# Optimization experiments

Hardware: AMD Instinct MI355X
Metric: run time of the kernel (lower is better)

## Reference

```python
import jax, jax.numpy as jnp
import numpy as np

S, B, D = 256, 256, 512
H, M = 512, 512

def setup_inputs() -> dict:
    key = jax.random.key(0)
    ks = jax.random.split(key, 5)
    scale = 0.05
    return {
        "input": jax.random.normal(ks[0], (S, B, D), dtype=jnp.float32),
        "w_ih": jax.random.normal(ks[1], (3 * H, D), dtype=jnp.float32) * scale,
        "w_hh": jax.random.normal(ks[2], (3 * H, H), dtype=jnp.float32) * scale,
        "b_ih": jnp.zeros((3 * H,), dtype=jnp.float32),
        "b_hh": jnp.zeros((3 * H,), dtype=jnp.float32),
        "W1": jax.random.normal(ks[3], (M, H), dtype=jnp.float32) * scale,
        "b1": jnp.zeros((M,), dtype=jnp.float32),
        "W2": jax.random.normal(ks[4], (1, M), dtype=jnp.float32) * scale,
        "b2": jnp.zeros((1,), dtype=jnp.float32),
    }

def _gru_cell(x_t, h, w_ih, w_hh, b_ih, b_hh):
    # PyTorch GRUCell: gates ordered (r, z, n) along the 3H axis.
    gi = x_t @ w_ih.T + b_ih            # [B, 3H]
    gh = h @ w_hh.T + b_hh              # [B, 3H]
    i_r, i_z, i_n = jnp.split(gi, 3, axis=-1)
    h_r, h_z, h_n = jnp.split(gh, 3, axis=-1)
    r = jax.nn.sigmoid(i_r + h_r)
    z = jax.nn.sigmoid(i_z + h_z)
    n = jnp.tanh(i_n + r * h_n)
    return (1.0 - z) * n + z * h

def reference(input, w_ih, w_hh, b_ih, b_hh, W1, b1, W2, b2):
    seq_len, batch_size, _ = input.shape
    h0 = jnp.zeros((batch_size, w_hh.shape[1]), dtype=input.dtype)

    def step(h, x_t):
        h_new = _gru_cell(x_t, h, w_ih, w_hh, b_ih, b_hh)
        return h_new, None

    h_final, _ = jax.lax.scan(step, h0, input)
    out1 = jnp.tanh(h_final @ W1.T + b1)   # [B, M]
    value = jnp.tanh(out1 @ W2.T + b2)     # [B, 1]
    return value
```

## Files before the change

### kernel.cpp

```cpp
#include <hip/hip_runtime.h>
#include <hip/hip_bf16.h>

typedef __attribute__((ext_vector_type(8))) short short8v;
typedef __attribute__((ext_vector_type(4))) float f32x4;

union SV { short8v v; unsigned short u[8]; };
union FU { float f; unsigned u; };
union QF { unsigned long long q[4]; float4 v[2]; };

__device__ __forceinline__ void split2(float x, unsigned short& hi, unsigned short& lo) {
    FU a; a.f = x;
    hi = (unsigned short)(a.u >> 16);
    FU h; h.u = a.u & 0xffff0000u;
    FU r; r.f = x - h.f;
    lo = (unsigned short)(r.u >> 16);
}
__device__ __forceinline__ void split8(const float4 a0, const float4 a1, SV& h, SV& l) {
    split2(a0.x, h.u[0], l.u[0]); split2(a0.y, h.u[1], l.u[1]);
    split2(a0.z, h.u[2], l.u[2]); split2(a0.w, h.u[3], l.u[3]);
    split2(a1.x, h.u[4], l.u[4]); split2(a1.y, h.u[5], l.u[5]);
    split2(a1.z, h.u[6], l.u[6]); split2(a1.w, h.u[7], l.u[7]);
}
__device__ __forceinline__ float sigmoidf_(float x) {
    return 1.0f / (1.0f + __expf(-x));
}

__device__ __forceinline__ unsigned long long h_load64(const float* p) {
    return __hip_atomic_load((const unsigned long long*)p,
                             __ATOMIC_RELAXED, __HIP_MEMORY_SCOPE_AGENT);
}
__device__ __forceinline__ float h_load32(const float* p) {
    FU u; u.u = __hip_atomic_load((const unsigned*)p,
                                  __ATOMIC_RELAXED, __HIP_MEMORY_SCOPE_AGENT);
    return u.f;
}
__device__ __forceinline__ void h_store32(float* p, float v) {
    FU u; u.f = v;
    __hip_atomic_store((unsigned*)p, u.u,
                       __ATOMIC_RELAXED, __HIP_MEMORY_SCOPE_AGENT);
}

__device__ __forceinline__ void group_barrier(unsigned* gf, const int ct,
                                              const unsigned gen) {
    __builtin_amdgcn_s_waitcnt(0);
    __syncthreads();
    __atomic_signal_fence(__ATOMIC_SEQ_CST);
    if (threadIdx.x == 0)
        __hip_atomic_store(&gf[ct], gen,
                           __ATOMIC_RELAXED, __HIP_MEMORY_SCOPE_AGENT);
    if (threadIdx.x < 16) {
        const unsigned long long* f64 = (const unsigned long long*)gf;
        for (;;) {
            unsigned long long v = __hip_atomic_load(
                &f64[threadIdx.x], __ATOMIC_RELAXED, __HIP_MEMORY_SCOPE_AGENT);
            if (((unsigned)v >= gen) && ((unsigned)(v >> 32) >= gen)) break;
            __builtin_amdgcn_s_sleep(1);
        }
    }
    __atomic_signal_fence(__ATOMIC_SEQ_CST);
    __syncthreads();
}

__global__ __launch_bounds__(256) void cast_split(
    const float* __restrict__ in, unsigned short* __restrict__ hi,
    unsigned short* __restrict__ lo, int n4)
{
    int i = blockIdx.x * 256 + threadIdx.x;
    if (i < n4) {
        float4 v = ((const float4*)in)[i];
        ushort4 h, l;
        split2(v.x, h.x, l.x); split2(v.y, h.y, l.y);
        split2(v.z, h.z, l.z); split2(v.w, h.w, l.w);
        ((ushort4*)hi)[i] = h;
        ((ushort4*)lo)[i] = l;
    }
}

__global__ __launch_bounds__(256, 2) void gemm_gi_mfma(
    const float* __restrict__ A,
    const unsigned short* __restrict__ Bh,
    const unsigned short* __restrict__ Bl,
    const float* __restrict__ bias,
    float* __restrict__ C)
{
    __shared__ __attribute__((aligned(16))) unsigned char lds[65536];
    const int t = threadIdx.x;
    const int l = t & 63, w = t >> 6;
    const int nb = blockIdx.x, mb = blockIdx.y;
    const int p = t & 7;
    const int rbase = t >> 3;
    f32x4 acc[4][4] = {};

    for (int kk = 0; kk < 512; kk += 64) {
#pragma unroll
        for (int i = 0; i < 4; ++i) {
            const int r = i * 32 + rbase;
            const int q = p ^ (r & 7);
            const float* ga = A + (size_t)(mb * 128 + r) * 512 + kk + q * 8;
            SV ah, al;
            split8(*(const float4*)ga, *(const float4*)(ga + 4), ah, al);
            const int o = r * 128 + p * 16;
            *(short8v*)&lds[o] = ah.v;
            *(short8v*)&lds[16384 + o] = al.v;
            const size_t gb = (size_t)(nb * 128 + r) * 512 + kk + q * 8;
            *(short8v*)&lds[32768 + o] = *(const short8v*)(Bh + gb);
            *(short8v*)&lds[49152 + o] = *(const short8v*)(Bl + gb);
        }
        __syncthreads();
        const int mr0 = (w >> 1) * 64, nc0 = (w & 1) * 64;
#pragma unroll
        for (int kk2 = 0; kk2 < 2; ++kk2) {
            const int kap = kk2 * 4 + (l >> 4);
            short8v ah[4], al[4], bh[4], bl[4];
#pragma unroll
            for (int i = 0; i < 4; ++i) {
                const int row = mr0 + i * 16 + (l & 15);
                const int off = row * 128 + ((kap ^ (row & 7)) * 16);
                ah[i] = *(const short8v*)&lds[off];
                al[i] = *(const short8v*)&lds[16384 + off];
            }
#pragma unroll
            for (int j = 0; j < 4; ++j) {
                const int bn = nc0 + j * 16 + (l & 15);
                const int off = bn * 128 + ((kap ^ (bn & 7)) * 16);
                bh[j] = *(const short8v*)&lds[32768 + off];
                bl[j] = *(const short8v*)&lds[49152 + off];
            }
#pragma unroll
            for (int i = 0; i < 4; ++i)
#pragma unroll
                for (int j = 0; j < 4; ++j) {
                    acc[i][j] = __builtin_amdgcn_mfma_f32_16x16x32_bf16(ah[i], bh[j], acc[i][j], 0, 0, 0);
                    acc[i][j] = __builtin_amdgcn_mfma_f32_16x16x32_bf16(ah[i], bl[j], acc[i][j], 0, 0, 0);
                    acc[i][j] = __builtin_amdgcn_mfma_f32_16x16x32_bf16(al[i], bh[j], acc[i][j], 0, 0, 0);
                }
        }
        __syncthreads();
    }
    const int mr0 = (w >> 1) * 64, nc0 = (w & 1) * 64;
#pragma unroll
    for (int j = 0; j < 4; ++j) {
        const int col = nb * 128 + nc0 + j * 16 + (l & 15);
        const float bv = bias[col];
#pragma unroll
        for (int i = 0; i < 4; ++i) {
            const int row0 = mb * 128 + mr0 + i * 16 + (l >> 4) * 4;
#pragma unroll
            for (int rg = 0; rg < 4; ++rg)
                C[(size_t)(row0 + rg) * 1536 + col] = acc[i][j][rg] + bv;
        }
    }
}

__device__ __forceinline__ void gru_tile_body(
    float* accs_f,
    const float* __restrict__ gi_s,
    const unsigned short* __restrict__ whhH,
    const unsigned short* __restrict__ whhL,
    const float* __restrict__ bhh,
    const float* __restrict__ hold,
    float* __restrict__ hnew,
    const int tid, const int rt, const int ct)
{
    const int l = tid & 63, wv = tid >> 6;
    const int c0 = ct * 16, row0 = rt * 16;
    const int arow = l & 15;
    const int ksl  = l >> 4;
    const int kbase = wv * 128;

    unsigned long long a_raw[4][4];
    const float* ha = hold + (size_t)(row0 + arow) * 512 + kbase + ksl * 8;
#pragma unroll
    for (int j = 0; j < 4; ++j)
#pragma unroll
        for (int q = 0; q < 4; ++q)
            a_raw[j][q] = h_load64(ha + j * 32 + q * 2);

    f32x4 acc[3] = {};
#pragma unroll
    for (int j = 0; j < 4; ++j) {
        QF buf;
#pragma unroll
        for (int q = 0; q < 4; ++q) buf.q[q] = a_raw[j][q];
        SV ah, al;
        split8(buf.v[0], buf.v[1], ah, al);
        const int ko = kbase + j * 32 + ksl * 8;
#pragma unroll
        for (int g = 0; g < 3; ++g) {
            const size_t wo = (size_t)((g << 9) + c0 + arow) * 512 + ko;
            const short8v bh = *(const short8v*)(whhH + wo);
            const short8v bl = *(const short8v*)(whhL + wo);
            acc[g] = __builtin_amdgcn_mfma_f32_16x16x32_bf16(ah.v, bh, acc[g], 0, 0, 0);
            acc[g] = __builtin_amdgcn_mfma_f32_16x16x32_bf16(ah.v, bl, acc[g], 0, 0, 0);
            acc[g] = __builtin_amdgcn_mfma_f32_16x16x32_bf16(al.v, bh, acc[g], 0, 0, 0);
        }
    }

#pragma unroll
    for (int g = 0; g < 3; ++g)
#pragma unroll
        for (int rg = 0; rg < 4; ++rg)
            accs_f[((wv * 3 + g) * 4 + rg) * 64 + l] = acc[g][rg];
    __syncthreads();

    const int col = c0 + arow;
    const int row = row0 + ((l >> 4) << 2) + wv;
    float s0 = accs_f[((0 * 3 + 0) * 4 + wv) * 64 + l]
             + accs_f[((1 * 3 + 0) * 4 + wv) * 64 + l]
             + accs_f[((2 * 3 + 0) * 4 + wv) * 64 + l]
             + accs_f[((3 * 3 + 0) * 4 + wv) * 64 + l];
    float s1 = accs_f[((0 * 3 + 1) * 4 + wv) * 64 + l]
             + accs_f[((1 * 3 + 1) * 4 + wv) * 64 + l]
             + accs_f[((2 * 3 + 1) * 4 + wv) * 64 + l]
             + accs_f[((3 * 3 + 1) * 4 + wv) * 64 + l];
    float s2 = accs_f[((0 * 3 + 2) * 4 + wv) * 64 + l]
             + accs_f[((1 * 3 + 2) * 4 + wv) * 64 + l]
             + accs_f[((2 * 3 + 2) * 4 + wv) * 64 + l]
             + accs_f[((3 * 3 + 2) * 4 + wv) * 64 + l];
    const float* gp = gi_s + (size_t)row * 1536 + col;
    const float hv = h_load32(hold + (size_t)row * 512 + col);
    const float r = sigmoidf_(gp[0]    + s0 + bhh[col]);
    const float z = sigmoidf_(gp[512]  + s1 + bhh[512 + col]);
    const float n = tanhf(gp[1024] + r * (s2 + bhh[1024 + col]));
    h_store32(hnew + (size_t)row * 512 + col, (1.0f - z) * n + z * hv);
    __syncthreads();
}

__global__ __launch_bounds__(256, 2) void gru_coop(
    const float* __restrict__ gi,
    const unsigned short* __restrict__ whhH,
    const unsigned short* __restrict__ whhL,
    const float* __restrict__ bhh,
    float* __restrict__ hA, float* __restrict__ hB,
    unsigned* __restrict__ flags,
    const int t0, const int tc)
{
    __shared__ float accs_f[4 * 3 * 4 * 64];
    const int tid = threadIdx.x;
    const int ct = blockIdx.x & 31;
    const int rt = blockIdx.x >> 5;
    unsigned* gf = flags + rt * 32;
    for (int s = 0; s < tc; ++s) {
        const int t = t0 + s;
        const float* hold = (t & 1) ? hB : hA;
        float* hnew = (t & 1) ? hA : hB;
        gru_tile_body(accs_f, gi + (size_t)s * 256 * 1536, whhH, whhL, bhh,
                      hold, hnew, tid, rt, ct);
        if (s + 1 < tc)
            group_barrier(gf, ct, (unsigned)(t + 1));
    }
}

__global__ __launch_bounds__(256, 2) void gru_step_fb(
    const float* __restrict__ gi_s,
    const unsigned short* __restrict__ whhH,
    const unsigned short* __restrict__ whhL,
    const float* __restrict__ bhh,
    const float* __restrict__ hold, float* __restrict__ hnew)
{
    __shared__ float accs_f[4 * 3 * 4 * 64];
    gru_tile_body(accs_f, gi_s, whhH, whhL, bhh, hold, hnew,
                  threadIdx.x, blockIdx.x >> 5, blockIdx.x & 31);
}

template<bool TANH>
__global__ __launch_bounds__(256) void gemm_nt_bias(
    const float* __restrict__ A, const float* __restrict__ B,
    const float* __restrict__ bias, float* __restrict__ C,
    const int N, const int K)
{
    __shared__ float As[32][68];
    __shared__ float Bs[32][68];
    const int nb = blockIdx.x, mb = blockIdx.y;
    const int t  = threadIdx.x;
    const int tx = t & 15, ty = t >> 4;
    const int lr = t >> 3;
    const int lk = (t & 7) << 2;
    const float* pA = A + (size_t)(mb * 64 + lr) * K + lk;
    const float* pB = B + (size_t)(nb * 64 + lr) * K + lk;
    float acc[4][4];
#pragma unroll
    for (int i = 0; i < 4; ++i)
#pragma unroll
        for (int j = 0; j < 4; ++j) acc[i][j] = 0.0f;
    for (int kk = 0; kk < K; kk += 32) {
        const float4 a0 = *(const float4*)(pA + kk);
        const float4 a1 = *(const float4*)(pA + (size_t)32 * K + kk);
        const float4 b0 = *(const float4*)(pB + kk);
        const float4 b1 = *(const float4*)(pB + (size_t)32 * K + kk);
        __syncthreads();
        As[lk+0][lr] = a0.x; As[lk+1][lr] = a0.y; As[lk+2][lr] = a0.z; As[lk+3][lr] = a0.w;
        As[lk+0][lr+32] = a1.x; As[lk+1][lr+32] = a1.y; As[lk+2][lr+32] = a1.z; As[lk+3][lr+32] = a1.w;
        Bs[lk+0][lr] = b0.x; Bs[lk+1][lr] = b0.y; Bs[lk+2][lr] = b0.z; Bs[lk+3][lr] = b0.w;
        Bs[lk+0][lr+32] = b1.x; Bs[lk+1][lr+32] = b1.y; Bs[lk+2][lr+32] = b1.z; Bs[lk+3][lr+32] = b1.w;
        __syncthreads();
#pragma unroll
        for (int k = 0; k < 32; ++k) {
            const float4 av = *(const float4*)&As[k][ty << 2];
            const float4 bv = *(const float4*)&Bs[k][tx << 2];
            acc[0][0] += av.x * bv.x; acc[0][1] += av.x * bv.y; acc[0][2] += av.x * bv.z; acc[0][3] += av.x * bv.w;
            acc[1][0] += av.y * bv.x; acc[1][1] += av.y * bv.y; acc[1][2] += av.y * bv.z; acc[1][3] += av.y * bv.w;
            acc[2][0] += av.z * bv.x; acc[2][1] += av.z * bv.y; acc[2][2] += av.z * bv.z; acc[2][3] += av.z * bv.w;
            acc[3][0] += av.w * bv.x; acc[3][1] += av.w * bv.y; acc[3][2] += av.w * bv.z; acc[3][3] += av.w * bv.w;
        }
    }
    const int crow = mb * 64 + (ty << 2);
    const int ccol = nb * 64 + (tx << 2);
    const float4 bv = *(const float4*)(bias + ccol);
#pragma unroll
    for (int i = 0; i < 4; ++i) {
        float4 o;
        o.x = acc[i][0] + bv.x; o.y = acc[i][1] + bv.y;
        o.z = acc[i][2] + bv.z; o.w = acc[i][3] + bv.w;
        if (TANH) { o.x = tanhf(o.x); o.y = tanhf(o.y); o.z = tanhf(o.z); o.w = tanhf(o.w); }
        *(float4*)(C + (size_t)(crow + i) * N + ccol) = o;
    }
}

__global__ __launch_bounds__(256) void value_head(
    const float* __restrict__ out1, const float* __restrict__ W2,
    const float* __restrict__ b2, float* __restrict__ out)
{
    const int b = blockIdx.x, t = threadIdx.x;
    float p = out1[(size_t)b * 512 + t] * W2[t]
            + out1[(size_t)b * 512 + 256 + t] * W2[256 + t];
#pragma unroll
    for (int off = 32; off > 0; off >>= 1) p += __shfl_down(p, off, 64);
    __shared__ float ps[4];
    if ((t & 63) == 0) ps[t >> 6] = p;
    __syncthreads();
    if (t == 0) out[b] = tanhf(ps[0] + ps[1] + ps[2] + ps[3] + b2[0]);
}

extern "C" void kernel_launch(void* const* d_in, const int* in_sizes, int n_in,
                              void* d_out, int out_size, void* d_ws, size_t ws_size,
                              hipStream_t stream)
{
    (void)in_sizes; (void)n_in; (void)out_size;
    const float* input = (const float*)d_in[0];
    const float* w_ih  = (const float*)d_in[1];
    const float* w_hh  = (const float*)d_in[2];
    const float* b_ih  = (const float*)d_in[3];
    const float* b_hh  = (const float*)d_in[4];
    const float* W1    = (const float*)d_in[5];
    const float* b1    = (const float*)d_in[6];
    const float* W2    = (const float*)d_in[7];
    const float* b2    = (const float*)d_in[8];
    float* out = (float*)d_out;
    float* ws  = (float*)d_ws;

    float* hA = ws;
    float* hB = ws + 131072;
    float* o1 = ws + 262144;
    unsigned short* wihH = (unsigned short*)(ws + 393216);
    unsigned short* wihL = (unsigned short*)(ws + 786432);
    unsigned short* whhH = (unsigned short*)(ws + 1179648);
    unsigned short* whhL = (unsigned short*)(ws + 1572864);
    unsigned* flags = (unsigned*)(ws + 1966080);
    float* gi = ws + 1966592;

    const size_t per_step = 256 * 1536;
    const size_t base = 1966592;
    const size_t avail = (ws_size / 4 > base) ? ws_size / 4 - base : 0;
    int Tc = (int)(avail / per_step);
    if (Tc > 256) Tc = 256;
    if (Tc < 1) Tc = 1;

    hipMemsetAsync(hA, 0, 131072 * sizeof(float), stream);
    hipMemsetAsync(flags, 0, 512 * sizeof(unsigned), stream);

    cast_split<<<768, 256, 0, stream>>>(w_ih, wihH, wihL, 196608);
    cast_split<<<768, 256, 0, stream>>>(w_hh, whhH, whhL, 196608);

    for (int t0 = 0; t0 < 256; t0 += Tc) {
        const int tc = (t0 + Tc <= 256) ? Tc : (256 - t0);
        const int Mc = tc * 256;
        gemm_gi_mfma<<<dim3(12, Mc / 128), 256, 0, stream>>>(
            input + (size_t)t0 * 256 * 512, wihH, wihL, b_ih, gi);
        {
            const float* a_gi = gi;
            const unsigned short* a_wh = whhH; const unsigned short* a_wl = whhL;
            const float* a_bh = b_hh;
            float* a_hA = hA; float* a_hB = hB;
            unsigned* a_fl = flags;
            int a_t0 = t0; int a_tc = tc;
            void* args[] = {&a_gi, &a_wh, &a_wl, &a_bh, &a_hA, &a_hB, &a_fl, &a_t0, &a_tc};
            hipError_t rc = hipLaunchCooperativeKernel(
                (const void*)gru_coop, dim3(512), dim3(256), args, 0, stream);
            if (rc != hipSuccess) {
                for (int s = 0; s < tc; ++s) {
                    const int t = t0 + s;
                    const float* hold = (t & 1) ? hB : hA;
                    float* hnew = (t & 1) ? hA : hB;
                    gru_step_fb<<<dim3(512), 256, 0, stream>>>(
                        gi + (size_t)s * per_step, whhH, whhL, b_hh, hold, hnew);
                }
            }
        }
    }

    gemm_nt_bias<true><<<dim3(512 / 64, 256 / 64), 256, 0, stream>>>(
        hA, W1, b1, o1, 512, 512);
    value_head<<<256, 256, 0, stream>>>(o1, W2, b2, out);
}
```

Baseline: 2.476 ms.

## Fuse input projection into cooperative GRU kernel, overlapping with the step barrier

Removes the separate gi GEMM and its large global gi buffer. The cooperative recurrent kernel now computes each tile's input-gate projection for step t+1 itself, right after writing h for step t and before waiting on the group barrier, so this independent work fills the barrier wait. It drops the gi write and read round trip through HBM but loses the efficient LDS-tiled GEMM. W_ih is now re-read every step from global memory, and each block performs extra MFMA work inside the serial loop.

```diff
diff --git a/kernel.cpp b/kernel.cpp
--- a/kernel.cpp
+++ b/kernel.cpp
@@ -76,97 +76,68 @@
     }
 }
 
-__global__ __launch_bounds__(256, 2) void gemm_gi_mfma(
-    const float* __restrict__ A,
-    const unsigned short* __restrict__ Bh,
-    const unsigned short* __restrict__ Bl,
-    const float* __restrict__ bias,
-    float* __restrict__ C)
-{
-    __shared__ __attribute__((aligned(16))) unsigned char lds[65536];
-    const int t = threadIdx.x;
-    const int l = t & 63, w = t >> 6;
-    const int nb = blockIdx.x, mb = blockIdx.y;
-    const int p = t & 7;
-    const int rbase = t >> 3;
-    f32x4 acc[4][4] = {};
-
-    for (int kk = 0; kk < 512; kk += 64) {
-#pragma unroll
-        for (int i = 0; i < 4; ++i) {
-            const int r = i * 32 + rbase;
-            const int q = p ^ (r & 7);
-            const float* ga = A + (size_t)(mb * 128 + r) * 512 + kk + q * 8;
-            SV ah, al;
-            split8(*(const float4*)ga, *(const float4*)(ga + 4), ah, al);
-            const int o = r * 128 + p * 16;
-            *(short8v*)&lds[o] = ah.v;
-            *(short8v*)&lds[16384 + o] = al.v;
-            const size_t gb = (size_t)(nb * 128 + r) * 512 + kk + q * 8;
-            *(short8v*)&lds[32768 + o] = *(const short8v*)(Bh + gb);
-            *(short8v*)&lds[49152 + o] = *(const short8v*)(Bl + gb);
-        }
-        __syncthreads();
-        const int mr0 = (w >> 1) * 64, nc0 = (w & 1) * 64;
-#pragma unroll
-        for (int kk2 = 0; kk2 < 2; ++kk2) {
-            const int kap = kk2 * 4 + (l >> 4);
-            short8v ah[4], al[4], bh[4], bl[4];
-#pragma unroll
-            for (int i = 0; i < 4; ++i) {
-                const int row = mr0 + i * 16 + (l & 15);
-                const int off = row * 128 + ((kap ^ (row & 7)) * 16);
-                ah[i] = *(const short8v*)&lds[off];
-                al[i] = *(const short8v*)&lds[16384 + off];
-            }
-#pragma unroll
-            for (int j = 0; j < 4; ++j) {
-                const int bn = nc0 + j * 16 + (l & 15);
-                const int off = bn * 128 + ((kap ^ (bn & 7)) * 16);
-                bh[j] = *(const short8v*)&lds[32768 + off];
-                bl[j] = *(const short8v*)&lds[49152 + off];
-            }
-#pragma unroll
-            for (int i = 0; i < 4; ++i)
-#pragma unroll
-                for (int j = 0; j < 4; ++j) {
-                    acc[i][j] = __builtin_amdgcn_mfma_f32_16x16x32_bf16(ah[i], bh[j], acc[i][j], 0, 0, 0);
-                    acc[i][j] = __builtin_amdgcn_mfma_f32_16x16x32_bf16(ah[i], bl[j], acc[i][j], 0, 0, 0);
-                    acc[i][j] = __builtin_amdgcn_mfma_f32_16x16x32_bf16(al[i], bh[j], acc[i][j], 0, 0, 0);
-                }
-        }
-        __syncthreads();
-    }
-    const int mr0 = (w >> 1) * 64, nc0 = (w & 1) * 64;
+__device__ __forceinline__ void gi_compute(
+    float* accs_g,
+    const float* __restrict__ X,
+    const unsigned short* __restrict__ wihH,
+    const unsigned short* __restrict__ wihL,
+    const int step, const int tid, const int rt, const int ct,
+    const float bir, const float biz, const float bin,
+    float& gr, float& gz, float& gn)
+{
+    const int l = tid & 63, wv = tid >> 6;
+    const int arow = l & 15, ksl = l >> 4, kbase = wv * 128;
+    const int c0 = ct * 16, row0 = rt * 16;
+    const float* xa = X + ((size_t)step * 256 + row0 + arow) * 512 + kbase + ksl * 8;
+    f32x4 acc[3] = {};
 #pragma unroll
     for (int j = 0; j < 4; ++j) {
-        const int col = nb * 128 + nc0 + j * 16 + (l & 15);
-        const float bv = bias[col];
-#pragma unroll
-        for (int i = 0; i < 4; ++i) {
-            const int row0 = mb * 128 + mr0 + i * 16 + (l >> 4) * 4;
-#pragma unroll
-            for (int rg = 0; rg < 4; ++rg)
-                C[(size_t)(row0 + rg) * 1536 + col] = acc[i][j][rg] + bv;
-        }
-    }
-}
-
-__device__ __forceinline__ void gru_tile_body(
-    float* accs_f,
-    const float* __restrict__ gi_s,
+        const float4 x0 = *(const float4*)(xa + j * 32);
+        const float4 x1 = *(const float4*)(xa + j * 32 + 4);
+        SV ah, al;
+        split8(x0, x1, ah, al);
+        const int ko = kbase + j * 32 + ksl * 8;
+#pragma unroll
+        for (int g = 0; g < 3; ++g) {
+            const size_t wo = (size_t)((g << 9) + c0 + arow) * 512 + ko;
+            const short8v bh = *(const short8v*)(wihH + wo);
+            const short8v bl = *(const short8v*)(wihL + wo);
+            acc[g] = __builtin_amdgcn_mfma_f32_16x16x32_bf16(ah.v, bh, acc[g], 0, 0, 0);
+            acc[g] = __builtin_amdgcn_mfma_f32_16x16x32_bf16(ah.v, bl, acc[g], 0, 0, 0);
+            acc[g] = __builtin_amdgcn_mfma_f32_16x16x32_bf16(al.v, bh, acc[g], 0, 0, 0);
+        }
+    }
+#pragma unroll
+    for (int g = 0; g < 3; ++g)
+#pragma unroll
+        for (int rg = 0; rg < 4; ++rg)
+            accs_g[((wv * 3 + g) * 4 + rg) * 64 + l] = acc[g][rg];
+    __syncthreads();
+    gr = accs_g[((0 * 3 + 0) * 4 + wv) * 64 + l]
+       + accs_g[((1 * 3 + 0) * 4 + wv) * 64 + l]
+       + accs_g[((2 * 3 + 0) * 4 + wv) * 64 + l]
+       + accs_g[((3 * 3 + 0) * 4 + wv) * 64 + l] + bir;
+    gz = accs_g[((0 * 3 + 1) * 4 + wv) * 64 + l]
+       + accs_g[((1 * 3 + 1) * 4 + wv) * 64 + l]
+       + accs_g[((2 * 3 + 1) * 4 + wv) * 64 + l]
+       + accs_g[((3 * 3 + 1) * 4 + wv) * 64 + l] + biz;
+    gn = accs_g[((0 * 3 + 2) * 4 + wv) * 64 + l]
+       + accs_g[((1 * 3 + 2) * 4 + wv) * 64 + l]
+       + accs_g[((2 * 3 + 2) * 4 + wv) * 64 + l]
+       + accs_g[((3 * 3 + 2) * 4 + wv) * 64 + l] + bin;
+}
+
+__device__ __forceinline__ void recur_compute(
+    float* accs_r,
     const unsigned short* __restrict__ whhH,
     const unsigned short* __restrict__ whhL,
-    const float* __restrict__ bhh,
     const float* __restrict__ hold,
-    float* __restrict__ hnew,
-    const int tid, const int rt, const int ct)
+    const int tid, const int rt, const int ct,
+    float& s0, float& s1, float& s2)
 {
     const int l = tid & 63, wv = tid >> 6;
+    const int arow = l & 15, ksl = l >> 4, kbase = wv * 128;
     const int c0 = ct * 16, row0 = rt * 16;
-    const int arow = l & 15;
-    const int ksl  = l >> 4;
-    const int kbase = wv * 128;
 
     unsigned long long a_raw[4][4];
     const float* ha = hold + (size_t)(row0 + arow) * 512 + kbase + ksl * 8;
@@ -195,72 +166,106 @@
             acc[g] = __builtin_amdgcn_mfma_f32_16x16x32_bf16(al.v, bh, acc[g], 0, 0, 0);
         }
     }
-
 #pragma unroll
     for (int g = 0; g < 3; ++g)
 #pragma unroll
         for (int rg = 0; rg < 4; ++rg)
-            accs_f[((wv * 3 + g) * 4 + rg) * 64 + l] = acc[g][rg];
-    __syncthreads();
-
-    const int col = c0 + arow;
-    const int row = row0 + ((l >> 4) << 2) + wv;
-    float s0 = accs_f[((0 * 3 + 0) * 4 + wv) * 64 + l]
-             + accs_f[((1 * 3 + 0) * 4 + wv) * 64 + l]
-             + accs_f[((2 * 3 + 0) * 4 + wv) * 64 + l]
-             + accs_f[((3 * 3 + 0) * 4 + wv) * 64 + l];
-    float s1 = accs_f[((0 * 3 + 1) * 4 + wv) * 64 + l]
-             + accs_f[((1 * 3 + 1) * 4 + wv) * 64 + l]
-             + accs_f[((2 * 3 + 1) * 4 + wv) * 64 + l]
-             + accs_f[((3 * 3 + 1) * 4 + wv) * 64 + l];
-    float s2 = accs_f[((0 * 3 + 2) * 4 + wv) * 64 + l]
-             + accs_f[((1 * 3 + 2) * 4 + wv) * 64 + l]
-             + accs_f[((2 * 3 + 2) * 4 + wv) * 64 + l]
-             + accs_f[((3 * 3 + 2) * 4 + wv) * 64 + l];
-    const float* gp = gi_s + (size_t)row * 1536 + col;
-    const float hv = h_load32(hold + (size_t)row * 512 + col);
-    const float r = sigmoidf_(gp[0]    + s0 + bhh[col]);
-    const float z = sigmoidf_(gp[512]  + s1 + bhh[512 + col]);
-    const float n = tanhf(gp[1024] + r * (s2 + bhh[1024 + col]));
-    h_store32(hnew + (size_t)row * 512 + col, (1.0f - z) * n + z * hv);
-    __syncthreads();
+            accs_r[((wv * 3 + g) * 4 + rg) * 64 + l] = acc[g][rg];
+    __syncthreads();
+    s0 = accs_r[((0 * 3 + 0) * 4 + wv) * 64 + l]
+       + accs_r[((1 * 3 + 0) * 4 + wv) * 64 + l]
+       + accs_r[((2 * 3 + 0) * 4 + wv) * 64 + l]
+       + accs_r[((3 * 3 + 0) * 4 + wv) * 64 + l];
+    s1 = accs_r[((0 * 3 + 1) * 4 + wv) * 64 + l]
+       + accs_r[((1 * 3 + 1) * 4 + wv) * 64 + l]
+       + accs_r[((2 * 3 + 1) * 4 + wv) * 64 + l]
+       + accs_r[((3 * 3 + 1) * 4 + wv) * 64 + l];
+    s2 = accs_r[((0 * 3 + 2) * 4 + wv) * 64 + l]
+       + accs_r[((1 * 3 + 2) * 4 + wv) * 64 + l]
+       + accs_r[((2 * 3 + 2) * 4 + wv) * 64 + l]
+       + accs_r[((3 * 3 + 2) * 4 + wv) * 64 + l];
 }
 
 __global__ __launch_bounds__(256, 2) void gru_coop(
-    const float* __restrict__ gi,
+    const float* __restrict__ X,
+    const unsigned short* __restrict__ wihH,
+    const unsigned short* __restrict__ wihL,
     const unsigned short* __restrict__ whhH,
     const unsigned short* __restrict__ whhL,
+    const float* __restrict__ bih,
     const float* __restrict__ bhh,
     float* __restrict__ hA, float* __restrict__ hB,
     unsigned* __restrict__ flags,
-    const int t0, const int tc)
-{
-    __shared__ float accs_f[4 * 3 * 4 * 64];
+    const int tc)
+{
+    __shared__ float accs_r[4 * 3 * 4 * 64];
+    __shared__ float accs_g[4 * 3 * 4 * 64];
     const int tid = threadIdx.x;
+    const int l = tid & 63, wv = tid >> 6;
     const int ct = blockIdx.x & 31;
     const int rt = blockIdx.x >> 5;
     unsigned* gf = flags + rt * 32;
-    for (int s = 0; s < tc; ++s) {
-        const int t = t0 + s;
+
+    const int col = ct * 16 + (l & 15);
+    const int row = rt * 16 + ((l >> 4) << 2) + wv;
+    const float bir = bih[col], biz = bih[512 + col], bin = bih[1024 + col];
+    const float bhr = bhh[col], bhz = bhh[512 + col], bhn = bhh[1024 + col];
+
+    float gir, giz, gin;
+    gi_compute(accs_g, X, wihH, wihL, 0, tid, rt, ct, bir, biz, bin,
+               gir, giz, gin);
+
+    for (int t = 0; t < tc; ++t) {
         const float* hold = (t & 1) ? hB : hA;
         float* hnew = (t & 1) ? hA : hB;
-        gru_tile_body(accs_f, gi + (size_t)s * 256 * 1536, whhH, whhL, bhh,
-                      hold, hnew, tid, rt, ct);
-        if (s + 1 < tc)
+
+        float s0, s1, s2;
+        recur_compute(accs_r, whhH, whhL, hold, tid, rt, ct, s0, s1, s2);
+
+        const float hv = h_load32(hold + (size_t)row * 512 + col);
+        const float r = sigmoidf_(gir + s0 + bhr);
+        const float z = sigmoidf_(giz + s1 + bhz);
+        const float n = tanhf(gin + r * (s2 + bhn));
+        h_store32(hnew + (size_t)row * 512 + col, (1.0f - z) * n + z * hv);
+
+        if (t + 1 < tc) {
+            gi_compute(accs_g, X, wihH, wihL, t + 1, tid, rt, ct,
+                       bir, biz, bin, gir, giz, gin);
             group_barrier(gf, ct, (unsigned)(t + 1));
+        }
     }
 }
 
 __global__ __launch_bounds__(256, 2) void gru_step_fb(
-    const float* __restrict__ gi_s,
+    const float* __restrict__ X,
+    const unsigned short* __restrict__ wihH,
+    const unsigned short* __restrict__ wihL,
     const unsigned short* __restrict__ whhH,
     const unsigned short* __restrict__ whhL,
+    const float* __restrict__ bih,
     const float* __restrict__ bhh,
-    const float* __restrict__ hold, float* __restrict__ hnew)
-{
-    __shared__ float accs_f[4 * 3 * 4 * 64];
-    gru_tile_body(accs_f, gi_s, whhH, whhL, bhh, hold, hnew,
-                  threadIdx.x, blockIdx.x >> 5, blockIdx.x & 31);
+    const float* __restrict__ hold, float* __restrict__ hnew,
+    const int step)
+{
+    __shared__ float accs_r[4 * 3 * 4 * 64];
+    __shared__ float accs_g[4 * 3 * 4 * 64];
+    const int tid = threadIdx.x;
+    const int l = tid & 63, wv = tid >> 6;
+    const int ct = blockIdx.x & 31;
+    const int rt = blockIdx.x >> 5;
+    const int col = ct * 16 + (l & 15);
+    const int row = rt * 16 + ((l >> 4) << 2) + wv;
+    const float bir = bih[col], biz = bih[512 + col], bin = bih[1024 + col];
+    float gir, giz, gin;
+    gi_compute(accs_g, X, wihH, wihL, step, tid, rt, ct, bir, biz, bin,
+               gir, giz, gin);
+    float s0, s1, s2;
+    recur_compute(accs_r, whhH, whhL, hold, tid, rt, ct, s0, s1, s2);
+    const float hv = h_load32(hold + (size_t)row * 512 + col);
+    const float r = sigmoidf_(gir + s0 + bhh[col]);
+    const float z = sigmoidf_(giz + s1 + bhh[512 + col]);
+    const float n = tanhf(gin + r * (s2 + bhh[1024 + col]));
+    h_store32(hnew + (size_t)row * 512 + col, (1.0f - z) * n + z * hv);
 }
 
 template<bool TANH>
@@ -336,7 +341,7 @@
                               void* d_out, int out_size, void* d_ws, size_t ws_size,
                               hipStream_t stream)
 {
-    (void)in_sizes; (void)n_in; (void)out_size;
+    (void)in_sizes; (void)n_in; (void)out_size; (void)ws_size;
     const float* input = (const float*)d_in[0];
     const float* w_ih  = (const float*)d_in[1];
     const float* w_hh  = (const float*)d_in[2];
@@ -357,44 +362,31 @@
     unsigned short* whhH = (unsigned short*)(ws + 1179648);
     unsigned short* whhL = (unsigned short*)(ws + 1572864);
     unsigned* flags = (unsigned*)(ws + 1966080);
-    float* gi = ws + 1966592;
-
-    const size_t per_step = 256 * 1536;
-    const size_t base = 1966592;
-    const size_t avail = (ws_size / 4 > base) ? ws_size / 4 - base : 0;
-    int Tc = (int)(avail / per_step);
-    if (Tc > 256) Tc = 256;
-    if (Tc < 1) Tc = 1;
-
-    hipMemsetAsync(hA, 0, 131072 * sizeof(float), stream);
+
+    hipMemsetAsync(hA, 0, 262144 * sizeof(float), stream);
     hipMemsetAsync(flags, 0, 512 * sizeof(unsigned), stream);
 
     cast_split<<<768, 256, 0, stream>>>(w_ih, wihH, wihL, 196608);
     cast_split<<<768, 256, 0, stream>>>(w_hh, whhH, whhL, 196608);
 
-    for (int t0 = 0; t0 < 256; t0 += Tc) {
-        const int tc = (t0 + Tc <= 256) ? Tc : (256 - t0);
-        const int Mc = tc * 256;
-        gemm_gi_mfma<<<dim3(12, Mc / 128), 256, 0, stream>>>(
-            input + (size_t)t0 * 256 * 512, wihH, wihL, b_ih, gi);
-        {
-            const float* a_gi = gi;
-            const unsigned short* a_wh = whhH; const unsigned short* a_wl = whhL;
-            const float* a_bh = b_hh;
-            float* a_hA = hA; float* a_hB = hB;
-            unsigned* a_fl = flags;
-            int a_t0 = t0; int a_tc = tc;
-            void* args[] = {&a_gi, &a_wh, &a_wl, &a_bh, &a_hA, &a_hB, &a_fl, &a_t0, &a_tc};
-            hipError_t rc = hipLaunchCooperativeKernel(
-                (const void*)gru_coop, dim3(512), dim3(256), args, 0, stream);
-            if (rc != hipSuccess) {
-                for (int s = 0; s < tc; ++s) {
-                    const int t = t0 + s;
-                    const float* hold = (t & 1) ? hB : hA;
-                    float* hnew = (t & 1) ? hA : hB;
-                    gru_step_fb<<<dim3(512), 256, 0, stream>>>(
-                        gi + (size_t)s * per_step, whhH, whhL, b_hh, hold, hnew);
-                }
+    {
+        const float* a_X = input;
+        const unsigned short* a_ih = wihH; const unsigned short* a_il = wihL;
+        const unsigned short* a_hh = whhH; const unsigned short* a_hl = whhL;
+        const float* a_bi = b_ih; const float* a_bh = b_hh;
+        float* a_hA = hA; float* a_hB = hB;
+        unsigned* a_fl = flags;
+        int a_tc = 256;
+        void* args[] = {&a_X, &a_ih, &a_il, &a_hh, &a_hl, &a_bi, &a_bh,
+                        &a_hA, &a_hB, &a_fl, &a_tc};
+        hipError_t rc = hipLaunchCooperativeKernel(
+            (const void*)gru_coop, dim3(512), dim3(256), args, 0, stream);
+        if (rc != hipSuccess) {
+            for (int t = 0; t < 256; ++t) {
+                const float* hold = (t & 1) ? hB : hA;
+                float* hnew = (t & 1) ? hA : hB;
+                gru_step_fb<<<dim3(512), 256, 0, stream>>>(
+                    input, wihH, wihL, whhH, whhL, b_ih, b_hh, hold, hnew, t);
             }
         }
     }
```

Result: slower. 3.620 ms (+46.2%).
